# Optimization experiments

Hardware: AMD Instinct MI355X
Metric: run time of the kernel (lower is better)

The kernel has to match this reference:

```python
import jax, jax.numpy as jnp
import numpy as np

INV_SQRT2 = 0.7071067811865476
SILU_SCALE = 1.0 / 0.6  # GemNet ScaledSiLU

def scaled_silu(x):
    return jax.nn.silu(x) * SILU_SCALE

def setup_inputs() -> dict:
    key = jax.random.key(0)
    ks = jax.random.split(key, 8)
    nAtoms, nEdges = 50000, 1000000
    dA, dE, dR, nHidden = 256, 256, 16, 3
    h = jax.random.normal(ks[0], (nAtoms, dA), dtype=jnp.float32)
    m = jax.random.normal(ks[1], (nEdges, dE), dtype=jnp.float32)
    rbf = jax.random.normal(ks[2], (nEdges, dR), dtype=jnp.float32)
    id_j = jax.random.randint(ks[3], (nEdges,), 0, nAtoms)
    W_rbf = jax.random.normal(ks[4], (dR, dE), dtype=jnp.float32) * 0.05
    W1 = jax.random.normal(ks[5], (dE, dA), dtype=jnp.float32) * 0.05
    res_W = jax.random.normal(ks[6], (nHidden, 2, dA, dA), dtype=jnp.float32) * 0.05
    scale = jnp.ones((1,), dtype=jnp.float32)
    return {"h": h, "m": m, "rbf": rbf, "id_j": id_j,
            "W_rbf": W_rbf, "W1": W1, "res_W": res_W, "scale": scale}

def reference(h, m, rbf, id_j, W_rbf, W1, res_W, scale):
    nAtoms = h.shape[0]
    # edge gate from RBF, elementwise scale of messages: [nEdges, dE]
    x = m * (rbf @ W_rbf)
    # scatter-sum edges -> atoms: [nAtoms, dE]
    x2 = jax.ops.segment_sum(x, id_j, num_segments=nAtoms)
    # ScalingFactor (fitted scalar)
    x = x2 * scale
    # Dense edge->atom with ScaledSiLU
    x = scaled_silu(x @ W1)
    # nHidden residual blocks, each = 2 Dense layers + residual, /sqrt(2)
    for i in range(res_W.shape[0]):
        y = scaled_silu(x @ res_W[i, 0])
        y = scaled_silu(y @ res_W[i, 1])
        x = (x + y) * INV_SQRT2
    return x
```

## Files before the change

kernel.cpp:

```cpp
#include <hip/hip_runtime.h>
#include <math.h>

#define INV_SQRT2f 0.70710678118654752440f
#define SILU_SCALEf (1.0f / 0.6f)

typedef __attribute__((ext_vector_type(8))) short bf16x8;
typedef __attribute__((ext_vector_type(4))) float f32x4;

__device__ __forceinline__ float ssilu(float v) {
    return (v / (1.0f + __expf(-v))) * SILU_SCALEf;
}

__device__ __forceinline__ unsigned short f2bf(float f) {
    unsigned int u = __float_as_uint(f);
    unsigned int r = (u + 0x7FFFu + ((u >> 16) & 1u)) >> 16;
    return (unsigned short)r;
}

__global__ void zero_kernel(int* __restrict__ p, int n)
{
    int i = blockIdx.x * blockDim.x + threadIdx.x;
    for (; i < n; i += gridDim.x * blockDim.x) p[i] = 0;
}

__global__ void hist_kernel(const int* __restrict__ id_j, int* __restrict__ counts,
                            int nEdges)
{
    int i = blockIdx.x * blockDim.x + threadIdx.x;
    for (; i < nEdges; i += gridDim.x * blockDim.x)
        atomicAdd(&counts[id_j[i]], 1);
}

__global__ void scan_reduce(const int* __restrict__ counts, int* __restrict__ bsum,
                            int n)
{
    __shared__ int s[256];
    int base = blockIdx.x * 1024;
    int t = threadIdx.x;
    int v = 0;
#pragma unroll
    for (int k = 0; k < 4; ++k) {
        int i = base + t + k * 256;
        if (i < n) v += counts[i];
    }
    s[t] = v;
    __syncthreads();
    for (int off = 128; off > 0; off >>= 1) {
        if (t < off) s[t] += s[t + off];
        __syncthreads();
    }
    if (t == 0) bsum[blockIdx.x] = s[0];
}

__global__ void scan_sums(int* __restrict__ bsum, int nb)
{
    int l = threadIdx.x & 63;
    int carry = 0;
    for (int base = 0; base < nb; base += 64) {
        int idx = base + l;
        int orig = (idx < nb) ? bsum[idx] : 0;
        int v = orig;
#pragma unroll
        for (int off = 1; off < 64; off <<= 1) {
            int u = __shfl_up(v, off, 64);
            if (l >= off) v += u;
        }
        if (idx < nb) bsum[idx] = carry + v - orig;
        carry += __shfl(v, 63, 64);
    }
}

__global__ void scan_write(const int* __restrict__ counts, const int* __restrict__ bsum,
                           int* __restrict__ offsets, int* __restrict__ cursor, int n)
{
    __shared__ int s[256];
    int base = blockIdx.x * 1024;
    int t = threadIdx.x;
    int v[4];
    int tot = 0;
#pragma unroll
    for (int k = 0; k < 4; ++k) {
        int i = base + t * 4 + k;
        int c = (i < n) ? counts[i] : 0;
        v[k] = tot; tot += c;
    }
    s[t] = tot;
    __syncthreads();
    for (int off = 1; off < 256; off <<= 1) {
        int x = (t >= off) ? s[t - off] : 0;
        __syncthreads();
        s[t] += x;
        __syncthreads();
    }
    int excl = (t > 0) ? s[t - 1] : 0;
    int bo = bsum[blockIdx.x];
#pragma unroll
    for (int k = 0; k < 4; ++k) {
        int i = base + t * 4 + k;
        if (i < n) { int o = bo + excl + v[k]; offsets[i] = o; cursor[i] = o; }
    }
}

__global__ void order_kernel(const int* __restrict__ id_j, int* __restrict__ cursor,
                             int* __restrict__ order, int nEdges)
{
    int i = blockIdx.x * blockDim.x + threadIdx.x;
    for (; i < nEdges; i += gridDim.x * blockDim.x) {
        int j = id_j[i];
        int p = atomicAdd(&cursor[j], 1);
        order[p] = i;
    }
}

__global__ void __launch_bounds__(256) gather_kernel(
    const float* __restrict__ m, const float* __restrict__ rbf,
    const int* __restrict__ order, const int* __restrict__ offsets,
    const int* __restrict__ counts, const float* __restrict__ W_rbf,
    float* __restrict__ x2)
{
    const int j = blockIdx.x;
    const int t = threadIdx.x;
    float w[16];
#pragma unroll
    for (int k = 0; k < 16; ++k) w[k] = W_rbf[k * 256 + t];

    const int s = offsets[j];
    const int n = counts[j];
    float acc = 0.0f;
    int i = 0;
    for (; i + 1 < n; i += 2) {
        int e0 = order[s + i], e1 = order[s + i + 1];
        const float4* r0 = reinterpret_cast<const float4*>(rbf + (long long)e0 * 16);
        const float4* r1 = reinterpret_cast<const float4*>(rbf + (long long)e1 * 16);
        float4 a0 = r0[0], b0 = r0[1], c0 = r0[2], d0 = r0[3];
        float4 a1 = r1[0], b1 = r1[1], c1 = r1[2], d1 = r1[3];
        float m0 = m[(long long)e0 * 256 + t];
        float m1 = m[(long long)e1 * 256 + t];
        float g0 = a0.x*w[0] + a0.y*w[1] + a0.z*w[2] + a0.w*w[3]
                 + b0.x*w[4] + b0.y*w[5] + b0.z*w[6] + b0.w*w[7]
                 + c0.x*w[8] + c0.y*w[9] + c0.z*w[10] + c0.w*w[11]
                 + d0.x*w[12] + d0.y*w[13] + d0.z*w[14] + d0.w*w[15];
        float g1 = a1.x*w[0] + a1.y*w[1] + a1.z*w[2] + a1.w*w[3]
                 + b1.x*w[4] + b1.y*w[5] + b1.z*w[6] + b1.w*w[7]
                 + c1.x*w[8] + c1.y*w[9] + c1.z*w[10] + c1.w*w[11]
                 + d1.x*w[12] + d1.y*w[13] + d1.z*w[14] + d1.w*w[15];
        acc += m0 * g0 + m1 * g1;
    }
    if (i < n) {
        int e0 = order[s + i];
        const float4* r0 = reinterpret_cast<const float4*>(rbf + (long long)e0 * 16);
        float4 a0 = r0[0], b0 = r0[1], c0 = r0[2], d0 = r0[3];
        float m0 = m[(long long)e0 * 256 + t];
        float g0 = a0.x*w[0] + a0.y*w[1] + a0.z*w[2] + a0.w*w[3]
                 + b0.x*w[4] + b0.y*w[5] + b0.z*w[6] + b0.w*w[7]
                 + c0.x*w[8] + c0.y*w[9] + c0.z*w[10] + c0.w*w[11]
                 + d0.x*w[12] + d0.y*w[13] + d0.z*w[14] + d0.w*w[15];
        acc += m0 * g0;
    }
    x2[(long long)j * 256 + t] = acc;
}

__global__ void __launch_bounds__(256) wconv_kernel(
    const float* __restrict__ W1, const float* __restrict__ res_W,
    unsigned short* __restrict__ blob)
{
    __shared__ float ws[32][260];
    const int b = blockIdx.x;
    const int L = b >> 3, c = b & 7;
    const int t = threadIdx.x;
    const float* W = (L == 0) ? W1 : res_W + (size_t)(L - 1) * 65536;

#pragma unroll
    for (int r = 0; r < 32; ++r)
        ws[r][t] = W[(size_t)(c * 32 + r) * 256 + t];
    __syncthreads();

    unsigned short* dst = blob + (size_t)b * 8192;
#pragma unroll
    for (int q = 0; q < 32; ++q) {
        int flat = q * 256 + t;
        int jj = flat & 7, n = (flat >> 3) & 255, g = flat >> 11;
        dst[flat] = f2bf(ws[g * 8 + jj][n]);
    }
}

__global__ void __launch_bounds__(512) dense_kernel(
    const float* __restrict__ x2, const unsigned short* __restrict__ blob,
    const float* __restrict__ scale, float* __restrict__ out, int nAtoms)
{
    __shared__ __align__(16) unsigned short xs[64 * 256];

    const int tid = threadIdx.x;
    const int lane = tid & 63;
    const int w = tid >> 6;
    const int l15 = lane & 15;
    const int g = lane >> 4;
    const long long blockRow = (long long)blockIdx.x * 64;

    {
        int row = tid >> 3;
        int c0 = (tid & 7) * 32;
        const float* src = x2 + (blockRow + row) * 256 + c0;
        int key = (row & 7) << 3;
#pragma unroll
        for (int i = 0; i < 4; ++i) {
            float4 a = *reinterpret_cast<const float4*>(src + i * 8);
            float4 b = *reinterpret_cast<const float4*>(src + i * 8 + 4);
            bf16x8 v = {(short)f2bf(a.x), (short)f2bf(a.y), (short)f2bf(a.z), (short)f2bf(a.w),
                        (short)f2bf(b.x), (short)f2bf(b.y), (short)f2bf(b.z), (short)f2bf(b.w)};
            int idx = (row * 256 + c0 + i * 8) ^ key;
            *reinterpret_cast<bf16x8*>(&xs[idx]) = v;
        }
    }

    const float sc = scale[0];
    f32x4 acc[4][2];
    float xrun[4][2][4];

    for (int L = 0; L < 7; ++L) {
        __syncthreads();

#pragma unroll
        for (int mt = 0; mt < 4; ++mt)
#pragma unroll
            for (int ct = 0; ct < 2; ++ct) acc[mt][ct] = (f32x4){0, 0, 0, 0};

        const unsigned short* wlayer = blob + (size_t)L * 65536;

        for (int c = 0; c < 8; ++c) {
            bf16x8 af[4], bfr[2];
#pragma unroll
            for (int mt = 0; mt < 4; ++mt) {
                int arow = mt * 16 + l15;
                int idx = (arow * 256 + c * 32 + g * 8) ^ ((arow & 7) << 3);
                af[mt] = *reinterpret_cast<const bf16x8*>(&xs[idx]);
            }
#pragma unroll
            for (int ct = 0; ct < 2; ++ct) {
                int n = w * 32 + ct * 16 + l15;
                bfr[ct] = *reinterpret_cast<const bf16x8*>(wlayer + ((size_t)c * 1024 + g * 256 + n) * 8);
            }
#pragma unroll
            for (int mt = 0; mt < 4; ++mt)
#pragma unroll
                for (int ct = 0; ct < 2; ++ct)
                    acc[mt][ct] = __builtin_amdgcn_mfma_f32_16x16x32_bf16(
                        af[mt], bfr[ct], acc[mt][ct], 0, 0, 0);
        }

        __syncthreads();

        if (L == 0) {
#pragma unroll
            for (int mt = 0; mt < 4; ++mt)
#pragma unroll
                for (int ct = 0; ct < 2; ++ct)
#pragma unroll
                    for (int r = 0; r < 4; ++r)
                        xrun[mt][ct][r] = ssilu(acc[mt][ct][r] * sc);
        } else if (L == 1 || L == 3 || L == 5) {
#pragma unroll
            for (int mt = 0; mt < 4; ++mt)
#pragma unroll
                for (int ct = 0; ct < 2; ++ct)
#pragma unroll
                    for (int r = 0; r < 4; ++r) {
                        float v = ssilu(acc[mt][ct][r]);
                        int row = mt * 16 + g * 4 + r;
                        int col = w * 32 + ct * 16 + l15;
                        xs[(row * 256 + col) ^ ((row & 7) << 3)] = f2bf(v);
                    }
            continue;
        } else {
#pragma unroll
            for (int mt = 0; mt < 4; ++mt)
#pragma unroll
                for (int ct = 0; ct < 2; ++ct)
#pragma unroll
                    for (int r = 0; r < 4; ++r)
                        xrun[mt][ct][r] = (xrun[mt][ct][r] + ssilu(acc[mt][ct][r])) * INV_SQRT2f;
        }

        if (L < 6) {
#pragma unroll
            for (int mt = 0; mt < 4; ++mt)
#pragma unroll
                for (int ct = 0; ct < 2; ++ct)
#pragma unroll
                    for (int r = 0; r < 4; ++r) {
                        int row = mt * 16 + g * 4 + r;
                        int col = w * 32 + ct * 16 + l15;
                        xs[(row * 256 + col) ^ ((row & 7) << 3)] = f2bf(xrun[mt][ct][r]);
                    }
        } else {
#pragma unroll
            for (int mt = 0; mt < 4; ++mt) {
#pragma unroll
                for (int r = 0; r < 4; ++r) {
                    long long grow = blockRow + mt * 16 + g * 4 + r;
                    if (grow < nAtoms) {
#pragma unroll
                        for (int ct = 0; ct < 2; ++ct)
                            out[grow * 256 + w * 32 + ct * 16 + l15] = xrun[mt][ct][r];
                    }
                }
            }
        }
    }
}

extern "C" void kernel_launch(void* const* d_in, const int* in_sizes, int n_in,
                              void* d_out, int out_size, void* d_ws, size_t ws_size,
                              hipStream_t stream)
{
    const float* m     = (const float*)d_in[1];
    const float* rbf   = (const float*)d_in[2];
    const int*   id_j  = (const int*)d_in[3];
    const float* W_rbf = (const float*)d_in[4];
    const float* W1    = (const float*)d_in[5];
    const float* res_W = (const float*)d_in[6];
    const float* scale = (const float*)d_in[7];

    const int nAtoms = in_sizes[0] / 256;
    const int nEdges = in_sizes[1] / 256;

    float* out = (float*)d_out;

    float* x2 = (float*)d_ws;
    unsigned short* blob = (unsigned short*)((char*)d_ws + 51249152);
    int* ibase   = (int*)((char*)d_ws + 52428800);
    int* counts  = ibase;
    int* offsets = ibase + 65536;
    int* cursor  = ibase + 131072;
    int* bsum    = ibase + 196608;
    int* order   = ibase + 197632;

    zero_kernel<<<64, 256, 0, stream>>>(counts, 65536);

    wconv_kernel<<<56, 256, 0, stream>>>(W1, res_W, blob);

    hist_kernel<<<2048, 256, 0, stream>>>(id_j, counts, nEdges);
    int nb = (nAtoms + 1023) / 1024;
    scan_reduce<<<nb, 256, 0, stream>>>(counts, bsum, nAtoms);
    scan_sums<<<1, 64, 0, stream>>>(bsum, nb);
    scan_write<<<nb, 256, 0, stream>>>(counts, bsum, offsets, cursor, nAtoms);
    order_kernel<<<2048, 256, 0, stream>>>(id_j, cursor, order, nEdges);
    gather_kernel<<<nAtoms, 256, 0, stream>>>(m, rbf, order, offsets, counts,
                                              W_rbf, x2);

    dense_kernel<<<(nAtoms + 63) / 64, 512, 0, stream>>>(x2, blob, scale, out, nAtoms);
}
```

Baseline: 581.6 us.

## Fuse edge gather-scatter into dense MLP kernel, removing x2 round trip

```diff
diff --git a/kernel.cpp b/kernel.cpp
--- a/kernel.cpp
+++ b/kernel.cpp
@@ -112,54 +112,6 @@
     }
 }
 
-__global__ void __launch_bounds__(256) gather_kernel(
-    const float* __restrict__ m, const float* __restrict__ rbf,
-    const int* __restrict__ order, const int* __restrict__ offsets,
-    const int* __restrict__ counts, const float* __restrict__ W_rbf,
-    float* __restrict__ x2)
-{
-    const int j = blockIdx.x;
-    const int t = threadIdx.x;
-    float w[16];
-#pragma unroll
-    for (int k = 0; k < 16; ++k) w[k] = W_rbf[k * 256 + t];
-
-    const int s = offsets[j];
-    const int n = counts[j];
-    float acc = 0.0f;
-    int i = 0;
-    for (; i + 1 < n; i += 2) {
-        int e0 = order[s + i], e1 = order[s + i + 1];
-        const float4* r0 = reinterpret_cast<const float4*>(rbf + (long long)e0 * 16);
-        const float4* r1 = reinterpret_cast<const float4*>(rbf + (long long)e1 * 16);
-        float4 a0 = r0[0], b0 = r0[1], c0 = r0[2], d0 = r0[3];
-        float4 a1 = r1[0], b1 = r1[1], c1 = r1[2], d1 = r1[3];
-        float m0 = m[(long long)e0 * 256 + t];
-        float m1 = m[(long long)e1 * 256 + t];
-        float g0 = a0.x*w[0] + a0.y*w[1] + a0.z*w[2] + a0.w*w[3]
-                 + b0.x*w[4] + b0.y*w[5] + b0.z*w[6] + b0.w*w[7]
-                 + c0.x*w[8] + c0.y*w[9] + c0.z*w[10] + c0.w*w[11]
-                 + d0.x*w[12] + d0.y*w[13] + d0.z*w[14] + d0.w*w[15];
-        float g1 = a1.x*w[0] + a1.y*w[1] + a1.z*w[2] + a1.w*w[3]
-                 + b1.x*w[4] + b1.y*w[5] + b1.z*w[6] + b1.w*w[7]
-                 + c1.x*w[8] + c1.y*w[9] + c1.z*w[10] + c1.w*w[11]
-                 + d1.x*w[12] + d1.y*w[13] + d1.z*w[14] + d1.w*w[15];
-        acc += m0 * g0 + m1 * g1;
-    }
-    if (i < n) {
-        int e0 = order[s + i];
-        const float4* r0 = reinterpret_cast<const float4*>(rbf + (long long)e0 * 16);
-        float4 a0 = r0[0], b0 = r0[1], c0 = r0[2], d0 = r0[3];
-        float m0 = m[(long long)e0 * 256 + t];
-        float g0 = a0.x*w[0] + a0.y*w[1] + a0.z*w[2] + a0.w*w[3]
-                 + b0.x*w[4] + b0.y*w[5] + b0.z*w[6] + b0.w*w[7]
-                 + c0.x*w[8] + c0.y*w[9] + c0.z*w[10] + c0.w*w[11]
-                 + d0.x*w[12] + d0.y*w[13] + d0.z*w[14] + d0.w*w[15];
-        acc += m0 * g0;
-    }
-    x2[(long long)j * 256 + t] = acc;
-}
-
 __global__ void __launch_bounds__(256) wconv_kernel(
     const float* __restrict__ W1, const float* __restrict__ res_W,
     unsigned short* __restrict__ blob)
@@ -184,34 +136,69 @@
     }
 }
 
-__global__ void __launch_bounds__(512) dense_kernel(
-    const float* __restrict__ x2, const unsigned short* __restrict__ blob,
+__global__ void __launch_bounds__(512, 4) fused_kernel(
+    const float* __restrict__ m, const float* __restrict__ rbf,
+    const int* __restrict__ order, const int* __restrict__ offsets,
+    const int* __restrict__ counts, const float* __restrict__ W_rbf,
+    const unsigned short* __restrict__ blob,
     const float* __restrict__ scale, float* __restrict__ out, int nAtoms)
 {
     __shared__ __align__(16) unsigned short xs[64 * 256];
 
     const int tid = threadIdx.x;
+    const long long blockRow = (long long)blockIdx.x * 64;
+
+    {
+        const int grp = tid >> 8;
+        const int u = tid & 255;
+        float w[16];
+#pragma unroll
+        for (int k = 0; k < 16; ++k) w[k] = W_rbf[k * 256 + u];
+
+        const int r0 = grp * 32;
+        for (int r = r0; r < r0 + 32; ++r) {
+            const long long j = blockRow + r;
+            int s = 0, n = 0;
+            if (j < nAtoms) { s = offsets[j]; n = counts[j]; }
+            float acc = 0.0f;
+            int i = 0;
+            for (; i + 1 < n; i += 2) {
+                int e0 = order[s + i], e1 = order[s + i + 1];
+                const float4* rp0 = reinterpret_cast<const float4*>(rbf + (long long)e0 * 16);
+                const float4* rp1 = reinterpret_cast<const float4*>(rbf + (long long)e1 * 16);
+                float4 a0 = rp0[0], b0 = rp0[1], c0 = rp0[2], d0 = rp0[3];
+                float4 a1 = rp1[0], b1 = rp1[1], c1 = rp1[2], d1 = rp1[3];
+                float m0 = m[(long long)e0 * 256 + u];
+                float m1 = m[(long long)e1 * 256 + u];
+                float g0 = a0.x*w[0] + a0.y*w[1] + a0.z*w[2] + a0.w*w[3]
+                         + b0.x*w[4] + b0.y*w[5] + b0.z*w[6] + b0.w*w[7]
+                         + c0.x*w[8] + c0.y*w[9] + c0.z*w[10] + c0.w*w[11]
+                         + d0.x*w[12] + d0.y*w[13] + d0.z*w[14] + d0.w*w[15];
+                float g1 = a1.x*w[0] + a1.y*w[1] + a1.z*w[2] + a1.w*w[3]
+                         + b1.x*w[4] + b1.y*w[5] + b1.z*w[6] + b1.w*w[7]
+                         + c1.x*w[8] + c1.y*w[9] + c1.z*w[10] + c1.w*w[11]
+                         + d1.x*w[12] + d1.y*w[13] + d1.z*w[14] + d1.w*w[15];
+                acc += m0 * g0 + m1 * g1;
+            }
+            if (i < n) {
+                int e0 = order[s + i];
+                const float4* rp0 = reinterpret_cast<const float4*>(rbf + (long long)e0 * 16);
+                float4 a0 = rp0[0], b0 = rp0[1], c0 = rp0[2], d0 = rp0[3];
+                float m0 = m[(long long)e0 * 256 + u];
+                float g0 = a0.x*w[0] + a0.y*w[1] + a0.z*w[2] + a0.w*w[3]
+                         + b0.x*w[4] + b0.y*w[5] + b0.z*w[6] + b0.w*w[7]
+                         + c0.x*w[8] + c0.y*w[9] + c0.z*w[10] + c0.w*w[11]
+                         + d0.x*w[12] + d0.y*w[13] + d0.z*w[14] + d0.w*w[15];
+                acc += m0 * g0;
+            }
+            xs[(r * 256 + u) ^ ((r & 7) << 3)] = f2bf(acc);
+        }
+    }
+
     const int lane = tid & 63;
-    const int w = tid >> 6;
+    const int wv = tid >> 6;
     const int l15 = lane & 15;
-    const int g = lane >> 4;
-    const long long blockRow = (long long)blockIdx.x * 64;
-
-    {
-        int row = tid >> 3;
-        int c0 = (tid & 7) * 32;
-        const float* src = x2 + (blockRow + row) * 256 + c0;
-        int key = (row & 7) << 3;
-#pragma unroll
-        for (int i = 0; i < 4; ++i) {
-            float4 a = *reinterpret_cast<const float4*>(src + i * 8);
-            float4 b = *reinterpret_cast<const float4*>(src + i * 8 + 4);
-            bf16x8 v = {(short)f2bf(a.x), (short)f2bf(a.y), (short)f2bf(a.z), (short)f2bf(a.w),
-                        (short)f2bf(b.x), (short)f2bf(b.y), (short)f2bf(b.z), (short)f2bf(b.w)};
-            int idx = (row * 256 + c0 + i * 8) ^ key;
-            *reinterpret_cast<bf16x8*>(&xs[idx]) = v;
-        }
-    }
+    const int g4 = lane >> 4;
 
     const float sc = scale[0];
     f32x4 acc[4][2];
@@ -232,13 +219,13 @@
 #pragma unroll
             for (int mt = 0; mt < 4; ++mt) {
                 int arow = mt * 16 + l15;
-                int idx = (arow * 256 + c * 32 + g * 8) ^ ((arow & 7) << 3);
+                int idx = (arow * 256 + c * 32 + g4 * 8) ^ ((arow & 7) << 3);
                 af[mt] = *reinterpret_cast<const bf16x8*>(&xs[idx]);
             }
 #pragma unroll
             for (int ct = 0; ct < 2; ++ct) {
-                int n = w * 32 + ct * 16 + l15;
-                bfr[ct] = *reinterpret_cast<const bf16x8*>(wlayer + ((size_t)c * 1024 + g * 256 + n) * 8);
+                int n = wv * 32 + ct * 16 + l15;
+                bfr[ct] = *reinterpret_cast<const bf16x8*>(wlayer + ((size_t)c * 1024 + g4 * 256 + n) * 8);
             }
 #pragma unroll
             for (int mt = 0; mt < 4; ++mt)
@@ -266,8 +253,8 @@
 #pragma unroll
                     for (int r = 0; r < 4; ++r) {
                         float v = ssilu(acc[mt][ct][r]);
-                        int row = mt * 16 + g * 4 + r;
-                        int col = w * 32 + ct * 16 + l15;
+                        int row = mt * 16 + g4 * 4 + r;
+                        int col = wv * 32 + ct * 16 + l15;
                         xs[(row * 256 + col) ^ ((row & 7) << 3)] = f2bf(v);
                     }
             continue;
@@ -288,8 +275,8 @@
                 for (int ct = 0; ct < 2; ++ct)
 #pragma unroll
                     for (int r = 0; r < 4; ++r) {
-                        int row = mt * 16 + g * 4 + r;
-                        int col = w * 32 + ct * 16 + l15;
+                        int row = mt * 16 + g4 * 4 + r;
+                        int col = wv * 32 + ct * 16 + l15;
                         xs[(row * 256 + col) ^ ((row & 7) << 3)] = f2bf(xrun[mt][ct][r]);
                     }
         } else {
@@ -297,11 +284,11 @@
             for (int mt = 0; mt < 4; ++mt) {
 #pragma unroll
                 for (int r = 0; r < 4; ++r) {
-                    long long grow = blockRow + mt * 16 + g * 4 + r;
+                    long long grow = blockRow + mt * 16 + g4 * 4 + r;
                     if (grow < nAtoms) {
 #pragma unroll
                         for (int ct = 0; ct < 2; ++ct)
-                            out[grow * 256 + w * 32 + ct * 16 + l15] = xrun[mt][ct][r];
+                            out[grow * 256 + wv * 32 + ct * 16 + l15] = xrun[mt][ct][r];
                     }
                 }
             }
@@ -326,9 +313,8 @@
 
     float* out = (float*)d_out;
 
-    float* x2 = (float*)d_ws;
-    unsigned short* blob = (unsigned short*)((char*)d_ws + 51249152);
-    int* ibase   = (int*)((char*)d_ws + 52428800);
+    unsigned short* blob = (unsigned short*)d_ws;
+    int* ibase   = (int*)((char*)d_ws + 1048576);
     int* counts  = ibase;
     int* offsets = ibase + 65536;
     int* cursor  = ibase + 131072;
@@ -345,8 +331,7 @@
     scan_sums<<<1, 64, 0, stream>>>(bsum, nb);
     scan_write<<<nb, 256, 0, stream>>>(counts, bsum, offsets, cursor, nAtoms);
     order_kernel<<<2048, 256, 0, stream>>>(id_j, cursor, order, nEdges);
-    gather_kernel<<<nAtoms, 256, 0, stream>>>(m, rbf, order, offsets, counts,
-                                              W_rbf, x2);
-
-    dense_kernel<<<(nAtoms + 63) / 64, 512, 0, stream>>>(x2, blob, scale, out, nAtoms);
-}
+
+    fused_kernel<<<(nAtoms + 63) / 64, 512, 0, stream>>>(
+        m, rbf, order, offsets, counts, W_rbf, blob, scale, out, nAtoms);
+}
```

Result: slower. 1.359 ms (+133.7%).

## Write gather output as swizzled bf16 tiles and load via global_load_lds

Applied to the files above, without the earlier changes.

```diff
diff --git a/kernel.cpp b/kernel.cpp
--- a/kernel.cpp
+++ b/kernel.cpp
@@ -112,54 +112,6 @@
     }
 }
 
-__global__ void __launch_bounds__(256) gather_kernel(
-    const float* __restrict__ m, const float* __restrict__ rbf,
-    const int* __restrict__ order, const int* __restrict__ offsets,
-    const int* __restrict__ counts, const float* __restrict__ W_rbf,
-    float* __restrict__ x2)
-{
-    const int j = blockIdx.x;
-    const int t = threadIdx.x;
-    float w[16];
-#pragma unroll
-    for (int k = 0; k < 16; ++k) w[k] = W_rbf[k * 256 + t];
-
-    const int s = offsets[j];
-    const int n = counts[j];
-    float acc = 0.0f;
-    int i = 0;
-    for (; i + 1 < n; i += 2) {
-        int e0 = order[s + i], e1 = order[s + i + 1];
-        const float4* r0 = reinterpret_cast<const float4*>(rbf + (long long)e0 * 16);
-        const float4* r1 = reinterpret_cast<const float4*>(rbf + (long long)e1 * 16);
-        float4 a0 = r0[0], b0 = r0[1], c0 = r0[2], d0 = r0[3];
-        float4 a1 = r1[0], b1 = r1[1], c1 = r1[2], d1 = r1[3];
-        float m0 = m[(long long)e0 * 256 + t];
-        float m1 = m[(long long)e1 * 256 + t];
-        float g0 = a0.x*w[0] + a0.y*w[1] + a0.z*w[2] + a0.w*w[3]
-                 + b0.x*w[4] + b0.y*w[5] + b0.z*w[6] + b0.w*w[7]
-                 + c0.x*w[8] + c0.y*w[9] + c0.z*w[10] + c0.w*w[11]
-                 + d0.x*w[12] + d0.y*w[13] + d0.z*w[14] + d0.w*w[15];
-        float g1 = a1.x*w[0] + a1.y*w[1] + a1.z*w[2] + a1.w*w[3]
-                 + b1.x*w[4] + b1.y*w[5] + b1.z*w[6] + b1.w*w[7]
-                 + c1.x*w[8] + c1.y*w[9] + c1.z*w[10] + c1.w*w[11]
-                 + d1.x*w[12] + d1.y*w[13] + d1.z*w[14] + d1.w*w[15];
-        acc += m0 * g0 + m1 * g1;
-    }
-    if (i < n) {
-        int e0 = order[s + i];
-        const float4* r0 = reinterpret_cast<const float4*>(rbf + (long long)e0 * 16);
-        float4 a0 = r0[0], b0 = r0[1], c0 = r0[2], d0 = r0[3];
-        float m0 = m[(long long)e0 * 256 + t];
-        float g0 = a0.x*w[0] + a0.y*w[1] + a0.z*w[2] + a0.w*w[3]
-                 + b0.x*w[4] + b0.y*w[5] + b0.z*w[6] + b0.w*w[7]
-                 + c0.x*w[8] + c0.y*w[9] + c0.z*w[10] + c0.w*w[11]
-                 + d0.x*w[12] + d0.y*w[13] + d0.z*w[14] + d0.w*w[15];
-        acc += m0 * g0;
-    }
-    x2[(long long)j * 256 + t] = acc;
-}
-
 __global__ void __launch_bounds__(256) wconv_kernel(
     const float* __restrict__ W1, const float* __restrict__ res_W,
     unsigned short* __restrict__ blob)
@@ -184,8 +136,57 @@
     }
 }
 
+__device__ __forceinline__ float dot16(const float* __restrict__ row,
+                                       const float* __restrict__ w)
+{
+    const float4* rp = reinterpret_cast<const float4*>(row);
+    float4 a = rp[0], b = rp[1], c = rp[2], d = rp[3];
+    return a.x*w[0] + a.y*w[1] + a.z*w[2] + a.w*w[3]
+         + b.x*w[4] + b.y*w[5] + b.z*w[6] + b.w*w[7]
+         + c.x*w[8] + c.y*w[9] + c.z*w[10] + c.w*w[11]
+         + d.x*w[12] + d.y*w[13] + d.z*w[14] + d.w*w[15];
+}
+
+__global__ void __launch_bounds__(256) gather_kernel(
+    const float* __restrict__ m, const float* __restrict__ rbf,
+    const int* __restrict__ order, const int* __restrict__ offsets,
+    const int* __restrict__ counts, const float* __restrict__ W_rbf,
+    unsigned short* __restrict__ x2b)
+{
+    const int j = blockIdx.x;
+    const int t = threadIdx.x;
+    float w[16];
+#pragma unroll
+    for (int k = 0; k < 16; ++k) w[k] = W_rbf[k * 256 + t];
+
+    const int s = offsets[j];
+    const int n = counts[j];
+    float acc = 0.0f;
+    int i = 0;
+    for (; i + 3 < n; i += 4) {
+        int e0 = order[s + i], e1 = order[s + i + 1];
+        int e2 = order[s + i + 2], e3 = order[s + i + 3];
+        float m0 = m[(long long)e0 * 256 + t];
+        float m1 = m[(long long)e1 * 256 + t];
+        float m2 = m[(long long)e2 * 256 + t];
+        float m3 = m[(long long)e3 * 256 + t];
+        float g0 = dot16(rbf + (long long)e0 * 16, w);
+        float g1 = dot16(rbf + (long long)e1 * 16, w);
+        float g2 = dot16(rbf + (long long)e2 * 16, w);
+        float g3 = dot16(rbf + (long long)e3 * 16, w);
+        acc += m0 * g0 + m1 * g1 + m2 * g2 + m3 * g3;
+    }
+    for (; i < n; ++i) {
+        int e0 = order[s + i];
+        acc += m[(long long)e0 * 256 + t] * dot16(rbf + (long long)e0 * 16, w);
+    }
+
+    const int tile = j >> 6, r = j & 63;
+    x2b[(size_t)tile * 16384 + ((r * 256 + t) ^ ((r & 7) << 3))] = f2bf(acc);
+}
+
 __global__ void __launch_bounds__(512) dense_kernel(
-    const float* __restrict__ x2, const unsigned short* __restrict__ blob,
+    const unsigned short* __restrict__ x2b, const unsigned short* __restrict__ blob,
     const float* __restrict__ scale, float* __restrict__ out, int nAtoms)
 {
     __shared__ __align__(16) unsigned short xs[64 * 256];
@@ -198,19 +199,16 @@
     const long long blockRow = (long long)blockIdx.x * 64;
 
     {
-        int row = tid >> 3;
-        int c0 = (tid & 7) * 32;
-        const float* src = x2 + (blockRow + row) * 256 + c0;
-        int key = (row & 7) << 3;
+        const char* gsrc = (const char*)(x2b + (size_t)blockIdx.x * 16384) + (size_t)tid * 16;
+        char* lbase = (char*)xs + w * 1024;
 #pragma unroll
         for (int i = 0; i < 4; ++i) {
-            float4 a = *reinterpret_cast<const float4*>(src + i * 8);
-            float4 b = *reinterpret_cast<const float4*>(src + i * 8 + 4);
-            bf16x8 v = {(short)f2bf(a.x), (short)f2bf(a.y), (short)f2bf(a.z), (short)f2bf(a.w),
-                        (short)f2bf(b.x), (short)f2bf(b.y), (short)f2bf(b.z), (short)f2bf(b.w)};
-            int idx = (row * 256 + c0 + i * 8) ^ key;
-            *reinterpret_cast<bf16x8*>(&xs[idx]) = v;
-        }
+            __builtin_amdgcn_global_load_lds(
+                (const __attribute__((address_space(1))) unsigned int*)(gsrc + i * 8192),
+                (__attribute__((address_space(3))) unsigned int*)(lbase + i * 8192),
+                16, 0, 0);
+        }
+        asm volatile("s_waitcnt vmcnt(0)" ::: "memory");
     }
 
     const float sc = scale[0];
@@ -326,9 +324,11 @@
 
     float* out = (float*)d_out;
 
-    float* x2 = (float*)d_ws;
-    unsigned short* blob = (unsigned short*)((char*)d_ws + 51249152);
-    int* ibase   = (int*)((char*)d_ws + 52428800);
+    const int nTiles = (nAtoms + 63) / 64;
+
+    unsigned short* x2b  = (unsigned short*)d_ws;
+    unsigned short* blob = (unsigned short*)((char*)d_ws + 25690112);
+    int* ibase   = (int*)((char*)d_ws + 26738688);
     int* counts  = ibase;
     int* offsets = ibase + 65536;
     int* cursor  = ibase + 131072;
@@ -345,8 +345,9 @@
     scan_sums<<<1, 64, 0, stream>>>(bsum, nb);
     scan_write<<<nb, 256, 0, stream>>>(counts, bsum, offsets, cursor, nAtoms);
     order_kernel<<<2048, 256, 0, stream>>>(id_j, cursor, order, nEdges);
+
     gather_kernel<<<nAtoms, 256, 0, stream>>>(m, rbf, order, offsets, counts,
-                                              W_rbf, x2);
-
-    dense_kernel<<<(nAtoms + 63) / 64, 512, 0, stream>>>(x2, blob, scale, out, nAtoms);
-}
+                                              W_rbf, x2b);
+
+    dense_kernel<<<nTiles, 512, 0, stream>>>(x2b, blob, scale, out, nAtoms);
+}
```

New measurement: 567.0 us. 1.03x faster.
